# Kernel optimization log

Measured on AMD Instinct MI355X. Metric: run time of the kernel, lower is better.

The kernel has to match this reference:

```python
import jax, jax.numpy as jnp
import numpy as np
import math

B, S, D, H = 4, 2048, 1024, 16
DH = D // H  # dim per head = 64


def setup_inputs() -> dict:
    key = jax.random.key(0)
    ks = jax.random.split(key, 12)
    scale = 0.02
    inp = {
        "query": jax.random.normal(ks[0], (B, S, D), jnp.float32),
        "key": jax.random.normal(ks[1], (B, S, D), jnp.float32),
        "value": jax.random.normal(ks[2], (B, S, D), jnp.float32),
        "mask": jnp.zeros((B, S), jnp.float32),  # additive mask, 0 = attend
        "Wq": jax.random.normal(ks[3], (D, D), jnp.float32) * scale,
        "bq": jnp.zeros((D,), jnp.float32),
        "Wk": jax.random.normal(ks[4], (D, D), jnp.float32) * scale,
        "bk": jnp.zeros((D,), jnp.float32),
        "Wv": jax.random.normal(ks[5], (D, D), jnp.float32) * scale,
        "bv": jnp.zeros((D,), jnp.float32),
        "Wo": jax.random.normal(ks[6], (D, D), jnp.float32) * scale,
        "bo": jnp.zeros((D,), jnp.float32),
    }
    return inp


def reference(query, key, value, mask, Wq, bq, Wk, bk, Wv, bv, Wo, bo):
    # Linear projections (torch Linear: x @ W.T + b; here W stored as (in, out))
    def shape(x):  # (B,S,D) -> (B,H,S,DH)
        return x.reshape(B, S, H, DH).transpose(0, 2, 1, 3)

    q = shape(query @ Wq + bq) / math.sqrt(DH)
    k = shape(key @ Wk + bk)
    v = shape(value @ Wv + bv)

    # scores: (B,H,S,S)
    scores = jnp.einsum("bhqd,bhkd->bhqk", q, k)
    scores = scores + mask[:, None, None, :]  # additive mask broadcast
    weights = jax.nn.softmax(scores, axis=-1)
    # dropout omitted (eval mode / p effectively 0 for reference)
    context = jnp.einsum("bhqk,bhkd->bhqd", weights, v)
    context = context.transpose(0, 2, 1, 3).reshape(B, S, D)
    out = context @ Wo + bo
    return out
```

## Files before the change

### kernel.cpp

```cpp
#include <hip/hip_runtime.h>
#include <hip/hip_bf16.h>

#define B_  4
#define S_  2048
#define D_  1024
#define H_  16
#define DH_ 64
#define M_  (B_*S_)

typedef __attribute__((ext_vector_type(8)))  short    bf16x8;
typedef __attribute__((ext_vector_type(4)))  float    f32x4;
typedef __attribute__((ext_vector_type(16))) float    f32x16;
typedef __attribute__((ext_vector_type(2)))  unsigned u32x2;

#define LOG2E 1.4426950408889634f

__device__ __forceinline__ void g2l16(const void* g, void* l) {
    __builtin_amdgcn_global_load_lds(
        (const __attribute__((address_space(1))) unsigned*)g,
        (__attribute__((address_space(3))) unsigned*)l, 16, 0, 0);
}

__global__ __launch_bounds__(256) void cvt_bf16_3(
    const float* __restrict__ x0, const float* __restrict__ x1, const float* __restrict__ x2,
    __hip_bfloat16* __restrict__ y0, __hip_bfloat16* __restrict__ y1, __hip_bfloat16* __restrict__ y2)
{
    const float* x = blockIdx.y == 0 ? x0 : (blockIdx.y == 1 ? x1 : x2);
    __hip_bfloat16* y = blockIdx.y == 0 ? y0 : (blockIdx.y == 1 ? y1 : y2);
    size_t i = ((size_t)blockIdx.x * 256 + threadIdx.x) * 8;
    float4 a = *(const float4*)(x + i);
    float4 b = *(const float4*)(x + i + 4);
    __hip_bfloat16 h[8];
    h[0] = __float2bfloat16(a.x); h[1] = __float2bfloat16(a.y);
    h[2] = __float2bfloat16(a.z); h[3] = __float2bfloat16(a.w);
    h[4] = __float2bfloat16(b.x); h[5] = __float2bfloat16(b.y);
    h[6] = __float2bfloat16(b.z); h[7] = __float2bfloat16(b.w);
    *(bf16x8*)(y + i) = *(const bf16x8*)h;
}

__global__ __launch_bounds__(256) void wtrans4(
    const float* __restrict__ W0, const float* __restrict__ W1,
    const float* __restrict__ W2, const float* __restrict__ W3,
    __hip_bfloat16* __restrict__ T0, __hip_bfloat16* __restrict__ T1,
    __hip_bfloat16* __restrict__ T2, __hip_bfloat16* __restrict__ T3)
{
    const float* W = blockIdx.z == 0 ? W0 : (blockIdx.z == 1 ? W1 : (blockIdx.z == 2 ? W2 : W3));
    __hip_bfloat16* Wt = blockIdx.z == 0 ? T0 : (blockIdx.z == 1 ? T1 : (blockIdx.z == 2 ? T2 : T3));
    __shared__ float t[32][33];
    const int bx = blockIdx.x * 32;
    const int by = blockIdx.y * 32;
    const int tx = threadIdx.x, ty = threadIdx.y;
    #pragma unroll
    for (int i = 0; i < 32; i += 8)
        t[ty + i][tx] = W[(size_t)(by + ty + i) * D_ + bx + tx];
    __syncthreads();
    #pragma unroll
    for (int i = 0; i < 32; i += 8)
        Wt[(size_t)(bx + ty + i) * D_ + by + tx] = __float2bfloat16(t[tx][ty + i]);
}

template<int OUT>
__global__ __launch_bounds__(256, 3) void gemm_bf16(
    const __hip_bfloat16* __restrict__ X, const __hip_bfloat16* __restrict__ Wt,
    const float* __restrict__ bias, void* __restrict__ Yv, float scale)
{
    __shared__ char Ab[16384];
    __shared__ char Bb[16384];

    const int tid = threadIdx.x;
    const int m0 = blockIdx.y * 128, n0 = blockIdx.x * 128;
    const int w = tid >> 6, l = tid & 63;
    const int wm = w >> 1, wn = w & 1;
    const int li = l & 15, lg = l >> 4;

    f32x4 acc[4][4];
    #pragma unroll
    for (int a = 0; a < 4; ++a)
        #pragma unroll
        for (int b = 0; b < 4; ++b)
            acc[a][b] = (f32x4){0.f, 0.f, 0.f, 0.f};

    for (int k0 = 0; k0 < D_; k0 += 64) {
        #pragma unroll
        for (int p = 0; p < 4; ++p) {
            int sl = p * 256 + tid;
            int row = sl >> 3, s = sl & 7;
            g2l16(X  + (size_t)(m0 + row) * D_ + k0 + s * 8, Ab + sl * 16);
            g2l16(Wt + (size_t)(n0 + row) * D_ + k0 + s * 8, Bb + sl * 16);
        }
        asm volatile("s_waitcnt vmcnt(0)");
        __syncthreads();

        #pragma unroll
        for (int kh = 0; kh < 2; ++kh) {
            bf16x8 af[4], bfr[4];
            #pragma unroll
            for (int mt = 0; mt < 4; ++mt)
                af[mt] = *(const bf16x8*)(Ab + (wm * 64 + mt * 16 + li) * 128 + kh * 64 + lg * 16);
            #pragma unroll
            for (int nt = 0; nt < 4; ++nt)
                bfr[nt] = *(const bf16x8*)(Bb + (wn * 64 + nt * 16 + li) * 128 + kh * 64 + lg * 16);
            #pragma unroll
            for (int mt = 0; mt < 4; ++mt)
                #pragma unroll
                for (int nt = 0; nt < 4; ++nt)
                    acc[mt][nt] = __builtin_amdgcn_mfma_f32_16x16x32_bf16(
                        af[mt], bfr[nt], acc[mt][nt], 0, 0, 0);
        }
        __syncthreads();
    }

    #pragma unroll
    for (int mt = 0; mt < 4; ++mt) {
        #pragma unroll
        for (int nt = 0; nt < 4; ++nt) {
            int col = n0 + wn * 64 + nt * 16 + li;
            float bv = bias[col];
            #pragma unroll
            for (int i = 0; i < 4; ++i) {
                int row = m0 + wm * 64 + mt * 16 + lg * 4 + i;
                float v = (acc[mt][nt][i] + bv) * scale;
                if (OUT == 0) {
                    ((__hip_bfloat16*)Yv)[(size_t)row * D_ + col] = __float2bfloat16(v);
                } else if (OUT == 1) {
                    int b = row >> 11, s = row & (S_ - 1);
                    int h = col >> 6,  dh = col & 63;
                    ((__hip_bfloat16*)Yv)[((((size_t)b * H_ + h) * DH_ + dh) << 11) + s] =
                        __float2bfloat16(v);
                } else {
                    ((float*)Yv)[(size_t)row * D_ + col] = v;
                }
            }
        }
    }
}

__global__ __launch_bounds__(512, 4) void attn_mfma(
    const __hip_bfloat16* __restrict__ q, const __hip_bfloat16* __restrict__ k,
    const __hip_bfloat16* __restrict__ vt, const float* __restrict__ mask,
    __hip_bfloat16* __restrict__ ctx)
{
    __shared__ char Kb[2][8192];
    __shared__ char Vb[2][8192];
    __shared__ float mlds[S_];

    const int tid = threadIdx.x;
    const int w = tid >> 6, l = tid & 63;
    const int q31 = l & 31, hi = l >> 5;
    const int bh = blockIdx.y, bb = bh >> 4, hh = bh & 15;
    const int q0 = blockIdx.x * 256;

    const __hip_bfloat16* kbase = k  + (size_t)bb * S_ * D_ + hh * 64;
    const __hip_bfloat16* vbase = vt + (size_t)bh * (DH_ * S_);

    for (int i = tid; i < S_ / 4; i += 512) {
        float4 mv = ((const float4*)(mask + (size_t)bb * S_))[i];
        mv.x *= LOG2E; mv.y *= LOG2E; mv.z *= LOG2E; mv.w *= LOG2E;
        ((float4*)mlds)[i] = mv;
    }

    const int qrow = q0 + w * 32 + q31;
    const __hip_bfloat16* qp = q + (size_t)(bb * S_ + qrow) * D_ + hh * 64;
    bf16x8 qf[4];
    #pragma unroll
    for (int mf = 0; mf < 4; ++mf)
        qf[mf] = *(const bf16x8*)(qp + mf * 16 + hi * 8);

    f32x16 ot0, ot1;
    #pragma unroll
    for (int r = 0; r < 16; ++r) { ot0[r] = 0.f; ot1[r] = 0.f; }
    float mrun = -1e30f, lsum = 0.f;

    {
        int sl = tid, row = sl >> 3, s = sl & 7, sw = s ^ (row & 7);
        g2l16(kbase + (size_t)row * D_ + sw * 8, Kb[0] + sl * 16);
        g2l16(vbase + (size_t)row * S_ + sw * 8, Vb[0] + sl * 16);
    }
    asm volatile("s_waitcnt vmcnt(0)");
    __syncthreads();

    int cur = 0;
    for (int kt = 0; kt < S_; kt += 64) {
        if (kt + 64 < S_) {
            int sl = tid, row = sl >> 3, s = sl & 7, sw = s ^ (row & 7);
            g2l16(kbase + (size_t)(kt + 64 + row) * D_ + sw * 8, Kb[cur ^ 1] + sl * 16);
            g2l16(vbase + (size_t)row * S_ + (kt + 64) + sw * 8, Vb[cur ^ 1] + sl * 16);
        }

        #pragma unroll
        for (int ks = 0; ks < 2; ++ks) {
            f32x16 sc;
            #pragma unroll
            for (int g = 0; g < 4; ++g) {
                f32x4 mq = *(const f32x4*)(mlds + kt + ks * 32 + g * 8 + hi * 4);
                sc[g * 4 + 0] = mq[0]; sc[g * 4 + 1] = mq[1];
                sc[g * 4 + 2] = mq[2]; sc[g * 4 + 3] = mq[3];
            }
            const int arow = ks * 32 + q31;
            #pragma unroll
            for (int mf = 0; mf < 4; ++mf) {
                int slot = (mf * 2 + hi) ^ (arow & 7);
                bf16x8 kf = *(const bf16x8*)(Kb[cur] + arow * 128 + slot * 16);
                sc = __builtin_amdgcn_mfma_f32_32x32x16_bf16(kf, qf[mf], sc, 0, 0, 0);
            }
            float a0 = fmaxf(sc[0], sc[1]),   a1 = fmaxf(sc[2], sc[3]);
            float a2 = fmaxf(sc[4], sc[5]),   a3 = fmaxf(sc[6], sc[7]);
            float a4 = fmaxf(sc[8], sc[9]),   a5 = fmaxf(sc[10], sc[11]);
            float a6 = fmaxf(sc[12], sc[13]), a7 = fmaxf(sc[14], sc[15]);
            float mt = fmaxf(fmaxf(fmaxf(a0, a1), fmaxf(a2, a3)),
                             fmaxf(fmaxf(a4, a5), fmaxf(a6, a7)));
            if (!__all(mt <= mrun + 8.0f)) {
                float mo = fmaxf(mt, __shfl_xor(mt, 32));
                float mnew = fmaxf(mrun, mo);
                float al = __builtin_amdgcn_exp2f(mrun - mnew);
                lsum *= al;
                #pragma unroll
                for (int r = 0; r < 16; ++r) { ot0[r] *= al; ot1[r] *= al; }
                mrun = mnew;
            }
            float ps[4] = {0.f, 0.f, 0.f, 0.f};
            #pragma unroll
            for (int r = 0; r < 16; ++r) {
                float e = __builtin_amdgcn_exp2f(sc[r] - mrun);
                sc[r] = e;
                ps[r & 3] += e;
            }
            lsum += (ps[0] + ps[1]) + (ps[2] + ps[3]);

            unsigned pw[8];
            #pragma unroll
            for (int m = 0; m < 8; ++m) {
                float lo = sc[2 * m], hp = sc[2 * m + 1];
                unsigned r_;
                asm("v_cvt_pk_bf16_f32 %0, %1, %2" : "=v"(r_) : "v"(lo), "v"(hp));
                pw[m] = r_;
            }
            u32x2 s02 = __builtin_amdgcn_permlane32_swap(pw[0], pw[2], false, false);
            u32x2 s13 = __builtin_amdgcn_permlane32_swap(pw[1], pw[3], false, false);
            u32x2 s46 = __builtin_amdgcn_permlane32_swap(pw[4], pw[6], false, false);
            u32x2 s57 = __builtin_amdgcn_permlane32_swap(pw[5], pw[7], false, false);
            union { unsigned u[4]; bf16x8 v; } pf0, pf1;
            pf0.u[0] = s02[0]; pf0.u[1] = s13[0]; pf0.u[2] = s02[1]; pf0.u[3] = s13[1];
            pf1.u[0] = s46[0]; pf1.u[1] = s57[0]; pf1.u[2] = s46[1]; pf1.u[3] = s57[1];

            #pragma unroll
            for (int kh = 0; kh < 2; ++kh) {
                bf16x8 pf = kh ? pf1.v : pf0.v;
                #pragma unroll
                for (int dt = 0; dt < 2; ++dt) {
                    int row = dt * 32 + q31;
                    int slot = (ks * 4 + kh * 2 + hi) ^ (row & 7);
                    bf16x8 vf = *(const bf16x8*)(Vb[cur] + row * 128 + slot * 16);
                    if (dt == 0)
                        ot0 = __builtin_amdgcn_mfma_f32_32x32x16_bf16(vf, pf, ot0, 0, 0, 0);
                    else
                        ot1 = __builtin_amdgcn_mfma_f32_32x32x16_bf16(vf, pf, ot1, 0, 0, 0);
                }
            }
        }
        asm volatile("s_waitcnt vmcnt(0)");
        __syncthreads();
        cur ^= 1;
    }

    float lt = lsum + __shfl_xor(lsum, 32);
    float inv = 1.0f / lt;
    __hip_bfloat16* cp = ctx + (size_t)(bb * S_ + qrow) * D_ + hh * 64;
    #pragma unroll
    for (int dt = 0; dt < 2; ++dt) {
        #pragma unroll
        for (int g = 0; g < 4; ++g) {
            float v0 = (dt ? ot1[g * 4 + 0] : ot0[g * 4 + 0]) * inv;
            float v1 = (dt ? ot1[g * 4 + 1] : ot0[g * 4 + 1]) * inv;
            float v2 = (dt ? ot1[g * 4 + 2] : ot0[g * 4 + 2]) * inv;
            float v3 = (dt ? ot1[g * 4 + 3] : ot0[g * 4 + 3]) * inv;
            unsigned w0, w1;
            asm("v_cvt_pk_bf16_f32 %0, %1, %2" : "=v"(w0) : "v"(v0), "v"(v1));
            asm("v_cvt_pk_bf16_f32 %0, %1, %2" : "=v"(w1) : "v"(v2), "v"(v3));
            u32x2 st; st[0] = w0; st[1] = w1;
            *(u32x2*)(cp + dt * 32 + g * 8 + hi * 4) = st;
        }
    }
}

extern "C" void kernel_launch(void* const* d_in, const int* in_sizes, int n_in,
                              void* d_out, int out_size, void* d_ws, size_t ws_size,
                              hipStream_t stream) {
    const float* query = (const float*)d_in[0];
    const float* key_  = (const float*)d_in[1];
    const float* value = (const float*)d_in[2];
    const float* mask  = (const float*)d_in[3];
    const float* Wq = (const float*)d_in[4];
    const float* bq = (const float*)d_in[5];
    const float* Wk = (const float*)d_in[6];
    const float* bk = (const float*)d_in[7];
    const float* Wv = (const float*)d_in[8];
    const float* bv = (const float*)d_in[9];
    const float* Wo = (const float*)d_in[10];
    const float* bo = (const float*)d_in[11];
    float* out = (float*)d_out;

    const size_t WSZ = (size_t)D_ * D_;
    const size_t ASZ = (size_t)M_ * D_;
    __hip_bfloat16* p   = (__hip_bfloat16*)d_ws;
    __hip_bfloat16* WtQ = p;            p += WSZ;
    __hip_bfloat16* WtK = p;            p += WSZ;
    __hip_bfloat16* WtV = p;            p += WSZ;
    __hip_bfloat16* WtO = p;            p += WSZ;
    __hip_bfloat16* Xq  = p;            p += ASZ;
    __hip_bfloat16* Xk  = p;            p += ASZ;
    __hip_bfloat16* Xv  = p;            p += ASZ;
    __hip_bfloat16* qb  = p;            p += ASZ;
    __hip_bfloat16* kb  = p;            p += ASZ;
    __hip_bfloat16* vtb = p;            p += ASZ;
    __hip_bfloat16* cb  = p;            p += ASZ;

    cvt_bf16_3<<<dim3(4096, 3), 256, 0, stream>>>(query, key_, value, Xq, Xk, Xv);
    wtrans4<<<dim3(32, 32, 4), dim3(32, 8), 0, stream>>>(Wq, Wk, Wv, Wo, WtQ, WtK, WtV, WtO);

    dim3 gg(D_ / 128, M_ / 128);
    gemm_bf16<0><<<gg, 256, 0, stream>>>(Xq, WtQ, bq, qb, 0.125f * LOG2E);
    gemm_bf16<0><<<gg, 256, 0, stream>>>(Xk, WtK, bk, kb, 1.0f);
    gemm_bf16<1><<<gg, 256, 0, stream>>>(Xv, WtV, bv, vtb, 1.0f);

    attn_mfma<<<dim3(S_ / 256, B_ * H_), 512, 0, stream>>>(qb, kb, vtb, mask, cb);

    gemm_bf16<2><<<gg, 256, 0, stream>>>(cb, WtO, bo, out, 1.0f);
}
```

Before: 238.6 us.

## Fuse fp32-to-bf16 conversion into batched QKV GEMM and retile attention

Drops the separate activation conversion kernel. The QKV GEMM now reads fp32 inputs directly, converts them in registers and stores bf16 into LDS, and runs all three projections in one launch via blockIdx.z. The attention kernel moves to 256-thread blocks covering 128 queries, with a remapped 1D grid that interleaves heads across blocks. It also adds s_setprio around the MFMA sections and restructures the max reduction. The cost targeted is the extra global round trip for converted activations plus launch overhead. In exchange, the A-tile load becomes synchronous register traffic instead of direct global-to-LDS loads, and the fp32 reads double the A bytes per tile.

```diff
diff --git a/kernel.cpp b/kernel.cpp
--- a/kernel.cpp
+++ b/kernel.cpp
@@ -19,23 +19,6 @@
     __builtin_amdgcn_global_load_lds(
         (const __attribute__((address_space(1))) unsigned*)g,
         (__attribute__((address_space(3))) unsigned*)l, 16, 0, 0);
-}
-
-__global__ __launch_bounds__(256) void cvt_bf16_3(
-    const float* __restrict__ x0, const float* __restrict__ x1, const float* __restrict__ x2,
-    __hip_bfloat16* __restrict__ y0, __hip_bfloat16* __restrict__ y1, __hip_bfloat16* __restrict__ y2)
-{
-    const float* x = blockIdx.y == 0 ? x0 : (blockIdx.y == 1 ? x1 : x2);
-    __hip_bfloat16* y = blockIdx.y == 0 ? y0 : (blockIdx.y == 1 ? y1 : y2);
-    size_t i = ((size_t)blockIdx.x * 256 + threadIdx.x) * 8;
-    float4 a = *(const float4*)(x + i);
-    float4 b = *(const float4*)(x + i + 4);
-    __hip_bfloat16 h[8];
-    h[0] = __float2bfloat16(a.x); h[1] = __float2bfloat16(a.y);
-    h[2] = __float2bfloat16(a.z); h[3] = __float2bfloat16(a.w);
-    h[4] = __float2bfloat16(b.x); h[5] = __float2bfloat16(b.y);
-    h[6] = __float2bfloat16(b.z); h[7] = __float2bfloat16(b.w);
-    *(bf16x8*)(y + i) = *(const bf16x8*)h;
 }
 
 __global__ __launch_bounds__(256) void wtrans4(
@@ -59,13 +42,23 @@
         Wt[(size_t)(bx + ty + i) * D_ + by + tx] = __float2bfloat16(t[tx][ty + i]);
 }
 
-template<int OUT>
-__global__ __launch_bounds__(256, 3) void gemm_bf16(
-    const __hip_bfloat16* __restrict__ X, const __hip_bfloat16* __restrict__ Wt,
-    const float* __restrict__ bias, void* __restrict__ Yv, float scale)
+__global__ __launch_bounds__(256, 3) void gemm_qkv(
+    const float* __restrict__ Xq, const float* __restrict__ Xk, const float* __restrict__ Xv,
+    const __hip_bfloat16* __restrict__ WtQ, const __hip_bfloat16* __restrict__ WtK,
+    const __hip_bfloat16* __restrict__ WtV,
+    const float* __restrict__ bq, const float* __restrict__ bk, const float* __restrict__ bv,
+    __hip_bfloat16* __restrict__ Yq, __hip_bfloat16* __restrict__ Yk,
+    __hip_bfloat16* __restrict__ Yv)
 {
     __shared__ char Ab[16384];
     __shared__ char Bb[16384];
+
+    const int bz = blockIdx.z;
+    const float* X = bz == 0 ? Xq : (bz == 1 ? Xk : Xv);
+    const __hip_bfloat16* Wt = bz == 0 ? WtQ : (bz == 1 ? WtK : WtV);
+    const float* bias = bz == 0 ? bq : (bz == 1 ? bk : bv);
+    __hip_bfloat16* Y = bz == 0 ? Yq : (bz == 1 ? Yk : Yv);
+    const float scale = bz == 0 ? 0.125f * LOG2E : 1.0f;
 
     const int tid = threadIdx.x;
     const int m0 = blockIdx.y * 128, n0 = blockIdx.x * 128;
@@ -85,8 +78,17 @@
         for (int p = 0; p < 4; ++p) {
             int sl = p * 256 + tid;
             int row = sl >> 3, s = sl & 7;
-            g2l16(X  + (size_t)(m0 + row) * D_ + k0 + s * 8, Ab + sl * 16);
             g2l16(Wt + (size_t)(n0 + row) * D_ + k0 + s * 8, Bb + sl * 16);
+        }
+        #pragma unroll
+        for (int p = 0; p < 8; ++p) {
+            int idx = p * 256 + tid;
+            int row = idx >> 4, c4 = idx & 15;
+            float4 xa = *(const float4*)(X + (size_t)(m0 + row) * D_ + k0 + c4 * 4);
+            union { __hip_bfloat16 h[4]; u32x2 u; } cv;
+            cv.h[0] = __float2bfloat16(xa.x); cv.h[1] = __float2bfloat16(xa.y);
+            cv.h[2] = __float2bfloat16(xa.z); cv.h[3] = __float2bfloat16(xa.w);
+            *(u32x2*)(Ab + row * 128 + c4 * 8) = cv.u;
         }
         asm volatile("s_waitcnt vmcnt(0)");
         __syncthreads();
@@ -115,27 +117,89 @@
         #pragma unroll
         for (int nt = 0; nt < 4; ++nt) {
             int col = n0 + wn * 64 + nt * 16 + li;
-            float bv = bias[col];
+            float bv_ = bias[col];
             #pragma unroll
             for (int i = 0; i < 4; ++i) {
                 int row = m0 + wm * 64 + mt * 16 + lg * 4 + i;
-                float v = (acc[mt][nt][i] + bv) * scale;
-                if (OUT == 0) {
-                    ((__hip_bfloat16*)Yv)[(size_t)row * D_ + col] = __float2bfloat16(v);
-                } else if (OUT == 1) {
+                float v = (acc[mt][nt][i] + bv_) * scale;
+                if (bz == 2) {
                     int b = row >> 11, s = row & (S_ - 1);
                     int h = col >> 6,  dh = col & 63;
-                    ((__hip_bfloat16*)Yv)[((((size_t)b * H_ + h) * DH_ + dh) << 11) + s] =
-                        __float2bfloat16(v);
+                    Y[((((size_t)b * H_ + h) * DH_ + dh) << 11) + s] = __float2bfloat16(v);
                 } else {
-                    ((float*)Yv)[(size_t)row * D_ + col] = v;
+                    Y[(size_t)row * D_ + col] = __float2bfloat16(v);
                 }
             }
         }
     }
 }
 
-__global__ __launch_bounds__(512, 4) void attn_mfma(
+__global__ __launch_bounds__(256, 3) void gemm_out(
+    const __hip_bfloat16* __restrict__ X, const __hip_bfloat16* __restrict__ Wt,
+    const float* __restrict__ bias, float* __restrict__ Y)
+{
+    __shared__ char Ab[16384];
+    __shared__ char Bb[16384];
+
+    const int tid = threadIdx.x;
+    const int m0 = blockIdx.y * 128, n0 = blockIdx.x * 128;
+    const int w = tid >> 6, l = tid & 63;
+    const int wm = w >> 1, wn = w & 1;
+    const int li = l & 15, lg = l >> 4;
+
+    f32x4 acc[4][4];
+    #pragma unroll
+    for (int a = 0; a < 4; ++a)
+        #pragma unroll
+        for (int b = 0; b < 4; ++b)
+            acc[a][b] = (f32x4){0.f, 0.f, 0.f, 0.f};
+
+    for (int k0 = 0; k0 < D_; k0 += 64) {
+        #pragma unroll
+        for (int p = 0; p < 4; ++p) {
+            int sl = p * 256 + tid;
+            int row = sl >> 3, s = sl & 7;
+            g2l16(X  + (size_t)(m0 + row) * D_ + k0 + s * 8, Ab + sl * 16);
+            g2l16(Wt + (size_t)(n0 + row) * D_ + k0 + s * 8, Bb + sl * 16);
+        }
+        asm volatile("s_waitcnt vmcnt(0)");
+        __syncthreads();
+
+        #pragma unroll
+        for (int kh = 0; kh < 2; ++kh) {
+            bf16x8 af[4], bfr[4];
+            #pragma unroll
+            for (int mt = 0; mt < 4; ++mt)
+                af[mt] = *(const bf16x8*)(Ab + (wm * 64 + mt * 16 + li) * 128 + kh * 64 + lg * 16);
+            #pragma unroll
+            for (int nt = 0; nt < 4; ++nt)
+                bfr[nt] = *(const bf16x8*)(Bb + (wn * 64 + nt * 16 + li) * 128 + kh * 64 + lg * 16);
+            #pragma unroll
+            for (int mt = 0; mt < 4; ++mt)
+                #pragma unroll
+                for (int nt = 0; nt < 4; ++nt)
+                    acc[mt][nt] = __builtin_amdgcn_mfma_f32_16x16x32_bf16(
+                        af[mt], bfr[nt], acc[mt][nt], 0, 0, 0);
+        }
+        __syncthreads();
+    }
+
+    #pragma unroll
+    for (int mt = 0; mt < 4; ++mt) {
+        #pragma unroll
+        for (int nt = 0; nt < 4; ++nt) {
+            int col = n0 + wn * 64 + nt * 16 + li;
+            float bv_ = bias[col];
+            #pragma unroll
+            for (int i = 0; i < 4; ++i) {
+                int row = m0 + wm * 64 + mt * 16 + lg * 4 + i;
+                Y[(size_t)row * D_ + col] = acc[mt][nt][i] + bv_;
+            }
+        }
+    }
+}
+
+__global__ __launch_bounds__(256, 4) void attn_mfma(
     const __hip_bfloat16* __restrict__ q, const __hip_bfloat16* __restrict__ k,
     const __hip_bfloat16* __restrict__ vt, const float* __restrict__ mask,
     __hip_bfloat16* __restrict__ ctx)
@@ -147,13 +211,17 @@
     const int tid = threadIdx.x;
     const int w = tid >> 6, l = tid & 63;
     const int q31 = l & 31, hi = l >> 5;
-    const int bh = blockIdx.y, bb = bh >> 4, hh = bh & 15;
-    const int q0 = blockIdx.x * 256;
+
+    const int bid = blockIdx.x;
+    const int j = bid >> 3;
+    const int bh = (bid & 7) * 8 + (j >> 4);
+    const int q0 = (j & 15) * 128;
+    const int bb = bh >> 4, hh = bh & 15;
 
     const __hip_bfloat16* kbase = k  + (size_t)bb * S_ * D_ + hh * 64;
     const __hip_bfloat16* vbase = vt + (size_t)bh * (DH_ * S_);
 
-    for (int i = tid; i < S_ / 4; i += 512) {
+    for (int i = tid; i < S_ / 4; i += 256) {
         float4 mv = ((const float4*)(mask + (size_t)bb * S_))[i];
         mv.x *= LOG2E; mv.y *= LOG2E; mv.z *= LOG2E; mv.w *= LOG2E;
         ((float4*)mlds)[i] = mv;
@@ -171,8 +239,9 @@
     for (int r = 0; r < 16; ++r) { ot0[r] = 0.f; ot1[r] = 0.f; }
     float mrun = -1e30f, lsum = 0.f;
 
-    {
-        int sl = tid, row = sl >> 3, s = sl & 7, sw = s ^ (row & 7);
+    #pragma unroll
+    for (int c = 0; c < 2; ++c) {
+        int sl = c * 256 + tid, row = sl >> 3, s = sl & 7, sw = s ^ (row & 7);
         g2l16(kbase + (size_t)row * D_ + sw * 8, Kb[0] + sl * 16);
         g2l16(vbase + (size_t)row * S_ + sw * 8, Vb[0] + sl * 16);
     }
@@ -182,9 +251,12 @@
     int cur = 0;
     for (int kt = 0; kt < S_; kt += 64) {
         if (kt + 64 < S_) {
-            int sl = tid, row = sl >> 3, s = sl & 7, sw = s ^ (row & 7);
-            g2l16(kbase + (size_t)(kt + 64 + row) * D_ + sw * 8, Kb[cur ^ 1] + sl * 16);
-            g2l16(vbase + (size_t)row * S_ + (kt + 64) + sw * 8, Vb[cur ^ 1] + sl * 16);
+            #pragma unroll
+            for (int c = 0; c < 2; ++c) {
+                int sl = c * 256 + tid, row = sl >> 3, s = sl & 7, sw = s ^ (row & 7);
+                g2l16(kbase + (size_t)(kt + 64 + row) * D_ + sw * 8, Kb[cur ^ 1] + sl * 16);
+                g2l16(vbase + (size_t)row * S_ + (kt + 64) + sw * 8, Vb[cur ^ 1] + sl * 16);
+            }
         }
 
         #pragma unroll
@@ -197,18 +269,20 @@
                 sc[g * 4 + 2] = mq[2]; sc[g * 4 + 3] = mq[3];
             }
             const int arow = ks * 32 + q31;
+            __builtin_amdgcn_s_setprio(1);
             #pragma unroll
             for (int mf = 0; mf < 4; ++mf) {
                 int slot = (mf * 2 + hi) ^ (arow & 7);
                 bf16x8 kf = *(const bf16x8*)(Kb[cur] + arow * 128 + slot * 16);
                 sc = __builtin_amdgcn_mfma_f32_32x32x16_bf16(kf, qf[mf], sc, 0, 0, 0);
             }
-            float a0 = fmaxf(sc[0], sc[1]),   a1 = fmaxf(sc[2], sc[3]);
-            float a2 = fmaxf(sc[4], sc[5]),   a3 = fmaxf(sc[6], sc[7]);
-            float a4 = fmaxf(sc[8], sc[9]),   a5 = fmaxf(sc[10], sc[11]);
-            float a6 = fmaxf(sc[12], sc[13]), a7 = fmaxf(sc[14], sc[15]);
-            float mt = fmaxf(fmaxf(fmaxf(a0, a1), fmaxf(a2, a3)),
-                             fmaxf(fmaxf(a4, a5), fmaxf(a6, a7)));
+            __builtin_amdgcn_s_setprio(0);
+            float t0 = fmaxf(fmaxf(sc[0], sc[1]), sc[2]);
+            float t1 = fmaxf(fmaxf(sc[3], sc[4]), sc[5]);
+            float t2 = fmaxf(fmaxf(sc[6], sc[7]), sc[8]);
+            float t3 = fmaxf(fmaxf(sc[9], sc[10]), sc[11]);
+            float t4 = fmaxf(fmaxf(sc[12], sc[13]), sc[14]);
+            float mt = fmaxf(fmaxf(fmaxf(t0, t1), t2), fmaxf(fmaxf(t3, t4), sc[15]));
             if (!__all(mt <= mrun + 8.0f)) {
                 float mo = fmaxf(mt, __shfl_xor(mt, 32));
                 float mnew = fmaxf(mrun, mo);
@@ -243,6 +317,7 @@
             pf0.u[0] = s02[0]; pf0.u[1] = s13[0]; pf0.u[2] = s02[1]; pf0.u[3] = s13[1];
             pf1.u[0] = s46[0]; pf1.u[1] = s57[0]; pf1.u[2] = s46[1]; pf1.u[3] = s57[1];
 
+            __builtin_amdgcn_s_setprio(1);
             #pragma unroll
             for (int kh = 0; kh < 2; ++kh) {
                 bf16x8 pf = kh ? pf1.v : pf0.v;
@@ -257,6 +332,7 @@
                         ot1 = __builtin_amdgcn_mfma_f32_32x32x16_bf16(vf, pf, ot1, 0, 0, 0);
                 }
             }
+            __builtin_amdgcn_s_setprio(0);
         }
         asm volatile("s_waitcnt vmcnt(0)");
         __syncthreads();
@@ -307,23 +383,17 @@
     __hip_bfloat16* WtK = p;            p += WSZ;
     __hip_bfloat16* WtV = p;            p += WSZ;
     __hip_bfloat16* WtO = p;            p += WSZ;
-    __hip_bfloat16* Xq  = p;            p += ASZ;
-    __hip_bfloat16* Xk  = p;            p += ASZ;
-    __hip_bfloat16* Xv  = p;            p += ASZ;
     __hip_bfloat16* qb  = p;            p += ASZ;
     __hip_bfloat16* kb  = p;            p += ASZ;
     __hip_bfloat16* vtb = p;            p += ASZ;
     __hip_bfloat16* cb  = p;            p += ASZ;
 
-    cvt_bf16_3<<<dim3(4096, 3), 256, 0, stream>>>(query, key_, value, Xq, Xk, Xv);
     wtrans4<<<dim3(32, 32, 4), dim3(32, 8), 0, stream>>>(Wq, Wk, Wv, Wo, WtQ, WtK, WtV, WtO);
 
-    dim3 gg(D_ / 128, M_ / 128);
-    gemm_bf16<0><<<gg, 256, 0, stream>>>(Xq, WtQ, bq, qb, 0.125f * LOG2E);
-    gemm_bf16<0><<<gg, 256, 0, stream>>>(Xk, WtK, bk, kb, 1.0f);
-    gemm_bf16<1><<<gg, 256, 0, stream>>>(Xv, WtV, bv, vtb, 1.0f);
-
-    attn_mfma<<<dim3(S_ / 256, B_ * H_), 512, 0, stream>>>(qb, kb, vtb, mask, cb);
-
-    gemm_bf16<2><<<gg, 256, 0, stream>>>(cb, WtO, bo, out, 1.0f);
-}
+    gemm_qkv<<<dim3(D_ / 128, M_ / 128, 3), 256, 0, stream>>>(
+        query, key_, value, WtQ, WtK, WtV, bq, bk, bv, qb, kb, vtb);
+
+    attn_mfma<<<dim3((S_ / 128) * B_ * H_), 256, 0, stream>>>(qb, kb, vtb, mask, cb);
+
+    gemm_out<<<dim3(D_ / 128, M_ / 128), 256, 0, stream>>>(cb, WtO, bo, out);
+}
```

After: 261.4 us. +9.5%, slower.
